# Optimization experiments

Hardware: AMD Instinct MI355X
Metric: run time of the kernel (lower is better)

The kernel has to match this reference:

```python
import jax, jax.numpy as jnp
import numpy as np

SHIFT = 1  # fixed value of the random shift_direction in the original __init__


def _unfold_k3(x, axis):
    """Extract length-3 patches (zero pad 1 each side) along `axis`.
    Inserts a new kernel axis of size 3 right after `axis` (c-major, kh-minor),
    matching torch.nn.functional.unfold channel ordering."""
    pad = [(0, 0)] * x.ndim
    pad[axis] = (1, 1)
    xp = jnp.pad(x, pad)
    L = x.shape[axis]
    sl = lambda i: jax.lax.slice_in_dim(xp, i, i + L, axis=axis)
    return jnp.stack([sl(0), sl(1), sl(2)], axis=axis)


def setup_inputs() -> dict:
    key = jax.random.key(0)
    k1, k2 = jax.random.split(key)
    x = jax.random.normal(k1, (1024, 64, 28, 28), dtype=jnp.float32)
    W = jax.random.normal(k2, (32, 3, 3, 128), dtype=jnp.float32)
    return {"x": x, "W": W}


def reference(x, W):
    # shift along width
    t = jnp.roll(x, SHIFT, axis=3)                        # (1024,64,28,28)
    # merge (C,H) -> pseudo-channel, unfold k=3 along original W (im2col #1)
    t = t.reshape(1024, 1792, 28)
    t = _unfold_k3(t, axis=2)                             # (1024,1792,3,28) = (n, c*h, kh, w)
    t = t.reshape(1024, 64, 28, 3, 28)                    # (n, c, h, kh, w)
    # split channels into 2 groups, interleave with w, shifted group-mix sum
    t = t.reshape(1024, 2, 32, 28, 3, 28)
    t = jnp.transpose(t, (0, 2, 3, 4, 5, 1))              # (n, 32, h, kh, w, 2)
    t = t.reshape(1024, 32, 28, 3, 56)
    t = jnp.roll(t, SHIFT, axis=4)
    t = t.reshape(1024, 32, 28, 3, 28, 2).sum(axis=5)     # (n, 32, h, kh, w)
    t = jnp.transpose(t, (0, 1, 2, 4, 3))                 # (n, 32, h, w, kh)
    # second unfold k=3 along h (im2col #2)
    t = t.reshape(1024, 32, 28, 84)                       # (n, 32, h, w*kh)
    t = _unfold_k3(t, axis=2)                             # (n, 32, kh2, h, w*kh)
    t = t.reshape(1024, 32, 3, 28, 28, 3)                 # (n, l, j, h, w, k)
    t = jnp.transpose(t, (0, 1, 3, 2, 4, 5))              # (m, l, n, j, o, k)
    # 3x3 conv as einsum: 32 in-ch -> 128 out-ch
    y = jnp.einsum('mlnjok,ljki->mnoi', t, W)             # (1024,28,28,128)
    return jnp.transpose(y, (0, 3, 1, 2))                 # (1024,128,28,28)
```

## Files before the change

kernel.cpp:

```cpp
#include <hip/hip_runtime.h>
#include <hip/hip_bf16.h>

typedef __attribute__((ext_vector_type(8))) short short8;
typedef __attribute__((ext_vector_type(4))) float float4v;

#define HH 28
#define WD 28
#define CIN 64
#define COUT 128
#define KTOT 288

__global__ __launch_bounds__(256) void prep_w_kernel(const float* __restrict__ W,
                                                     __hip_bfloat16* __restrict__ Wbf) {
    int idx = blockIdx.x * 256 + threadIdx.x;
    if (idx >= COUT * KTOT) return;
    int i = idx / KTOT;
    int K = idx - i * KTOT;
    int jk = K >> 5;
    int l = K & 31;
    int j = jk / 3;
    int k = jk - j * 3;
    Wbf[idx] = __float2bfloat16(W[((l * 3 + j) * 3 + k) * COUT + i]);
}

__global__ __launch_bounds__(256) void conv_kernel(const float* __restrict__ x,
                                                   const __hip_bfloat16* __restrict__ Wbf,
                                                   float* __restrict__ out) {
    __shared__ __align__(16) char Vb[30 * 30 * 64];
    __shared__ __align__(16) char V0b[30 * 3 * 64];

    const int m = blockIdx.x;
    const int tid = threadIdx.x;
    const float* xm = x + (size_t)m * (CIN * HH * WD);

    for (int idx = tid; idx < 30 * 4 * 32; idx += 256) {
        int a  = idx & 31;
        int lq = (idx >> 5) & 3;
        int rp = idx >> 7;
        if (a >= 30) continue;
        int r = rp - 1;
        bool rok = (r >= 0) && (r < HH);
        bool m1 = rok && (a < 28);
        bool m2 = rok && (a >= 1) && (a <= 28);
        int i1 = a - 1; if (i1 < 0) i1 += 28;
        int i2 = a - 2; if (i2 < 0) i2 += 28;
        const float* x1 = xm + ((lq * 8) * HH + r) * WD;
        const float* x2 = x1 + 32 * HH * WD;
        short8 sv;
#pragma unroll
        for (int c = 0; c < 8; ++c) {
            float t = 0.f;
            if (m1) t += x1[c * HH * WD + i1];
            if (m2) t += x2[c * HH * WD + i2];
            __hip_bfloat16 hb = __float2bfloat16(t);
            sv[c] = *reinterpret_cast<short*>(&hb);
        }
        unsigned byte = (unsigned)(rp * 30 + a) * 64 + (unsigned)lq * 16;
        byte ^= (byte >> 3) & 0x30;
        *(short8*)(Vb + byte) = sv;
    }

    for (int idx = tid; idx < 30 * 3 * 32; idx += 256) {
        int l = idx & 31;
        int t3 = idx >> 5;
        int k = t3 % 3;
        int rp = t3 / 3;
        int r = rp - 1;
        float v = 0.f;
        if (r >= 0 && r < HH) {
            const float* x1 = xm + (l * HH + r) * WD;
            const float* x2 = x1 + 32 * HH * WD;
            if (k == 0) v = x2[25];
            else if (k == 1) v = x1[27] + x2[26];
            else v = x1[0];
        }
        __hip_bfloat16 hb = __float2bfloat16(v);
        *(__hip_bfloat16*)(V0b + idx * 2) = hb;
    }
    __syncthreads();

    const int lane = tid & 63;
    const int wv = tid >> 6;
    const int row = lane & 15;
    const int q = lane >> 4;
    const unsigned qb = (unsigned)q * 16;

    short8 Areg[2][9];
#pragma unroll
    for (int mt = 0; mt < 2; ++mt) {
        const __hip_bfloat16* ap = Wbf + (wv * 32 + mt * 16 + row) * KTOT + q * 8;
#pragma unroll
        for (int s = 0; s < 9; ++s)
            Areg[mt][s] = *(const short8*)(ap + s * 32);
    }

    const bool spec0 = (row == 0);
    const bool spec1 = (row >= 12);

    for (int h = 0; h < HH; ++h) {
        float4v acc[2][2] = {};
#pragma unroll
        for (int s = 0; s < 9; ++s) {
            const int j = s / 3;
            const int k = s - j * 3;
            const int rp = h + j;
            int a0 = row + k - 1;
            unsigned b0 = (unsigned)((rp * 30 + a0) * 64) + qb;
            b0 ^= (b0 >> 3) & 0x30;
            const char* p0 = spec0 ? (V0b + (unsigned)(rp * 3 + k) * 64 + qb)
                                   : (Vb + b0);
            unsigned b1 = (unsigned)((rp * 30 + (row + 15 + k)) * 64) + qb;
            b1 ^= (b1 >> 3) & 0x30;
            const char* p1 = spec1 ? (V0b + qb) : (Vb + b1);

            short8 bfr0 = *(const short8*)p0;
            short8 bfr1 = *(const short8*)p1;

            acc[0][0] = __builtin_amdgcn_mfma_f32_16x16x32_bf16(Areg[0][s], bfr0, acc[0][0], 0, 0, 0);
            acc[1][0] = __builtin_amdgcn_mfma_f32_16x16x32_bf16(Areg[1][s], bfr0, acc[1][0], 0, 0, 0);
            acc[0][1] = __builtin_amdgcn_mfma_f32_16x16x32_bf16(Areg[0][s], bfr1, acc[0][1], 0, 0, 0);
            acc[1][1] = __builtin_amdgcn_mfma_f32_16x16x32_bf16(Areg[1][s], bfr1, acc[1][1], 0, 0, 0);
        }
#pragma unroll
        for (int mt = 0; mt < 2; ++mt) {
            const int ibase = wv * 32 + mt * 16 + q * 4;
            float* op0 = out + (((size_t)m * COUT + ibase) * HH + h) * WD;
#pragma unroll
            for (int rr = 0; rr < 4; ++rr) {
                op0[rr * (HH * WD) + row] = acc[mt][0][rr];
                if (row < 12) op0[rr * (HH * WD) + 16 + row] = acc[mt][1][rr];
            }
        }
    }
}

extern "C" void kernel_launch(void* const* d_in, const int* in_sizes, int n_in,
                              void* d_out, int out_size, void* d_ws, size_t ws_size,
                              hipStream_t stream) {
    const float* x = (const float*)d_in[0];
    const float* W = (const float*)d_in[1];
    float* out = (float*)d_out;
    __hip_bfloat16* Wbf = (__hip_bfloat16*)d_ws;

    prep_w_kernel<<<(COUT * KTOT + 255) / 256, 256, 0, stream>>>(W, Wbf);
    conv_kernel<<<1024, 256, 0, stream>>>(x, Wbf, out);
}
```

Baseline: 803.2 us.

## Split each image's rows across two blocks to shrink LDS and raise occupancy

Each block now handles 14 of the 28 output rows of one image, staging only the 16 padded input rows it needs, so LDS per block drops from about 63KB to about 34KB. This is meant to let more blocks fit per CU (launch bounds hint 4) and give the GPU twice as many blocks. The weight register load is hoisted above the LDS staging so its latency overlaps, and a small zero region replaces reuse of the V0 buffer for padding. The cost is redundant staging of the two halo rows per block and duplicated weight loads.

```diff
diff --git a/kernel.cpp b/kernel.cpp
--- a/kernel.cpp
+++ b/kernel.cpp
@@ -9,6 +9,11 @@
 #define CIN 64
 #define COUT 128
 #define KTOT 288
+#define HB 14
+#define RP 16
+#define V0OFF (RP * 30 * 64)
+#define ZOFF  (V0OFF + RP * 3 * 64)
+#define LDSZ  (ZOFF + 64)
 
 __global__ __launch_bounds__(256) void prep_w_kernel(const float* __restrict__ W,
                                                      __hip_bfloat16* __restrict__ Wbf) {
@@ -23,61 +28,15 @@
     Wbf[idx] = __float2bfloat16(W[((l * 3 + j) * 3 + k) * COUT + i]);
 }
 
-__global__ __launch_bounds__(256) void conv_kernel(const float* __restrict__ x,
-                                                   const __hip_bfloat16* __restrict__ Wbf,
-                                                   float* __restrict__ out) {
-    __shared__ __align__(16) char Vb[30 * 30 * 64];
-    __shared__ __align__(16) char V0b[30 * 3 * 64];
+__global__ __launch_bounds__(256, 4) void conv_kernel(const float* __restrict__ x,
+                                                      const __hip_bfloat16* __restrict__ Wbf,
+                                                      float* __restrict__ out) {
+    __shared__ __align__(16) char L[LDSZ];
 
-    const int m = blockIdx.x;
+    const int hb = blockIdx.x;
+    const int m  = blockIdx.y;
     const int tid = threadIdx.x;
     const float* xm = x + (size_t)m * (CIN * HH * WD);
-
-    for (int idx = tid; idx < 30 * 4 * 32; idx += 256) {
-        int a  = idx & 31;
-        int lq = (idx >> 5) & 3;
-        int rp = idx >> 7;
-        if (a >= 30) continue;
-        int r = rp - 1;
-        bool rok = (r >= 0) && (r < HH);
-        bool m1 = rok && (a < 28);
-        bool m2 = rok && (a >= 1) && (a <= 28);
-        int i1 = a - 1; if (i1 < 0) i1 += 28;
-        int i2 = a - 2; if (i2 < 0) i2 += 28;
-        const float* x1 = xm + ((lq * 8) * HH + r) * WD;
-        const float* x2 = x1 + 32 * HH * WD;
-        short8 sv;
-#pragma unroll
-        for (int c = 0; c < 8; ++c) {
-            float t = 0.f;
-            if (m1) t += x1[c * HH * WD + i1];
-            if (m2) t += x2[c * HH * WD + i2];
-            __hip_bfloat16 hb = __float2bfloat16(t);
-            sv[c] = *reinterpret_cast<short*>(&hb);
-        }
-        unsigned byte = (unsigned)(rp * 30 + a) * 64 + (unsigned)lq * 16;
-        byte ^= (byte >> 3) & 0x30;
-        *(short8*)(Vb + byte) = sv;
-    }
-
-    for (int idx = tid; idx < 30 * 3 * 32; idx += 256) {
-        int l = idx & 31;
-        int t3 = idx >> 5;
-        int k = t3 % 3;
-        int rp = t3 / 3;
-        int r = rp - 1;
-        float v = 0.f;
-        if (r >= 0 && r < HH) {
-            const float* x1 = xm + (l * HH + r) * WD;
-            const float* x2 = x1 + 32 * HH * WD;
-            if (k == 0) v = x2[25];
-            else if (k == 1) v = x1[27] + x2[26];
-            else v = x1[0];
-        }
-        __hip_bfloat16 hb = __float2bfloat16(v);
-        *(__hip_bfloat16*)(V0b + idx * 2) = hb;
-    }
-    __syncthreads();
 
     const int lane = tid & 63;
     const int wv = tid >> 6;
@@ -94,33 +53,82 @@
             Areg[mt][s] = *(const short8*)(ap + s * 32);
     }
 
+    if (tid < 16) *(float*)(L + ZOFF + tid * 4) = 0.f;
+
+    for (int idx = tid; idx < RP * 4 * 32; idx += 256) {
+        int a  = idx & 31;
+        int lq = (idx >> 5) & 3;
+        int rp = idx >> 7;
+        if (a < 30) {
+            int r = hb * HB + rp - 1;
+            bool rok = (r >= 0) && (r < HH);
+            bool m1 = rok && (a < 28);
+            bool m2 = rok && (a >= 1) && (a <= 28);
+            int i1 = a - 1; if (i1 < 0) i1 += 28;
+            int i2 = a - 2; if (i2 < 0) i2 += 28;
+            const float* x1 = xm + ((lq * 8) * HH + r) * WD;
+            const float* x2 = x1 + 32 * HH * WD;
+            short8 sv;
+#pragma unroll
+            for (int c = 0; c < 8; ++c) {
+                float t = 0.f;
+                if (m1) t += x1[c * HH * WD + i1];
+                if (m2) t += x2[c * HH * WD + i2];
+                __hip_bfloat16 hv = __float2bfloat16(t);
+                sv[c] = *reinterpret_cast<short*>(&hv);
+            }
+            unsigned byte = (unsigned)(rp * 30 + a) * 64 + (unsigned)lq * 16;
+            byte ^= (byte >> 3) & 0x30;
+            *(short8*)(L + byte) = sv;
+        }
+    }
+
+    for (int idx = tid; idx < RP * 3 * 32; idx += 256) {
+        int l = idx & 31;
+        int t3 = idx >> 5;
+        int k = t3 % 3;
+        int rp = t3 / 3;
+        int r = hb * HB + rp - 1;
+        float v = 0.f;
+        if (r >= 0 && r < HH) {
+            const float* x1 = xm + (l * HH + r) * WD;
+            const float* x2 = x1 + 32 * HH * WD;
+            if (k == 0) v = x2[25];
+            else if (k == 1) v = x1[27] + x2[26];
+            else v = x1[0];
+        }
+        __hip_bfloat16 hv = __float2bfloat16(v);
+        *(__hip_bfloat16*)(L + V0OFF + idx * 2) = hv;
+    }
+    __syncthreads();
+
     const bool spec0 = (row == 0);
     const bool spec1 = (row >= 12);
 
-    for (int h = 0; h < HH; ++h) {
+    for (int hl = 0; hl < HB; ++hl) {
         float4v acc[2][2] = {};
 #pragma unroll
         for (int s = 0; s < 9; ++s) {
             const int j = s / 3;
             const int k = s - j * 3;
-            const int rp = h + j;
+            const int rp = hl + j;
             int a0 = row + k - 1;
             unsigned b0 = (unsigned)((rp * 30 + a0) * 64) + qb;
             b0 ^= (b0 >> 3) & 0x30;
-            const char* p0 = spec0 ? (V0b + (unsigned)(rp * 3 + k) * 64 + qb)
-                                   : (Vb + b0);
+            unsigned off0 = spec0 ? (unsigned)(V0OFF + (rp * 3 + k) * 64) + qb : b0;
             unsigned b1 = (unsigned)((rp * 30 + (row + 15 + k)) * 64) + qb;
             b1 ^= (b1 >> 3) & 0x30;
-            const char* p1 = spec1 ? (V0b + qb) : (Vb + b1);
+            unsigned off1 = spec1 ? (unsigned)ZOFF + qb : b1;
 
-            short8 bfr0 = *(const short8*)p0;
-            short8 bfr1 = *(const short8*)p1;
+            short8 bfr0 = *(const short8*)(L + off0);
+            short8 bfr1 = *(const short8*)(L + off1);
 
             acc[0][0] = __builtin_amdgcn_mfma_f32_16x16x32_bf16(Areg[0][s], bfr0, acc[0][0], 0, 0, 0);
             acc[1][0] = __builtin_amdgcn_mfma_f32_16x16x32_bf16(Areg[1][s], bfr0, acc[1][0], 0, 0, 0);
             acc[0][1] = __builtin_amdgcn_mfma_f32_16x16x32_bf16(Areg[0][s], bfr1, acc[0][1], 0, 0, 0);
             acc[1][1] = __builtin_amdgcn_mfma_f32_16x16x32_bf16(Areg[1][s], bfr1, acc[1][1], 0, 0, 0);
         }
+        const int h = hb * HB + hl;
 #pragma unroll
         for (int mt = 0; mt < 2; ++mt) {
             const int ibase = wv * 32 + mt * 16 + q * 4;
@@ -143,5 +151,5 @@
     __hip_bfloat16* Wbf = (__hip_bfloat16*)d_ws;
 
     prep_w_kernel<<<(COUT * KTOT + 255) / 256, 256, 0, stream>>>(W, Wbf);
-    conv_kernel<<<1024, 256, 0, stream>>>(x, Wbf, out);
+    conv_kernel<<<dim3(2, 1024), 256, 0, stream>>>(x, Wbf, out);
 }
```

After: 749.1 us. -6.7%, faster.

## Stream input rows via async global-to-LDS loads into a rolling ring buffer

Applied to the files above, without the earlier changes.

Replaces the up-front staging of the whole 30x30 padded input tile with a 4-slot ring buffer. One wave issues async global_load_lds for upcoming input rows, and the other waves build the bf16 mixed rows from LDS a few rows ahead of the MFMA loop. This shrinks LDS use so more blocks fit per CU (launch bounds set to 4) and overlaps global loads with compute. The cost is a barrier per output row and a load-issuing wave whose stalls sit on the critical path.

```diff
diff --git a/kernel.cpp b/kernel.cpp
--- a/kernel.cpp
+++ b/kernel.cpp
@@ -9,6 +9,16 @@
 #define CIN 64
 #define COUT 128
 #define KTOT 288
+
+#define VOFF  0
+#define V0OFF 7680
+#define ZOFF  (V0OFF + 768)
+#define XOFF  (ZOFF + 64)
+#define XROW  7168
+#define LDSZ  (XOFF + 4 * XROW)
+
+typedef const __attribute__((address_space(1))) char gchar;
+typedef __attribute__((address_space(3))) char lchar;
 
 __global__ __launch_bounds__(256) void prep_w_kernel(const float* __restrict__ W,
                                                      __hip_bfloat16* __restrict__ Wbf) {
@@ -23,112 +33,150 @@
     Wbf[idx] = __float2bfloat16(W[((l * 3 + j) * 3 + k) * COUT + i]);
 }
 
-__global__ __launch_bounds__(256) void conv_kernel(const float* __restrict__ x,
-                                                   const __hip_bfloat16* __restrict__ Wbf,
-                                                   float* __restrict__ out) {
-    __shared__ __align__(16) char Vb[30 * 30 * 64];
-    __shared__ __align__(16) char V0b[30 * 3 * 64];
+__global__ __launch_bounds__(256, 4) void conv_kernel(const float* __restrict__ x,
+                                                      const __hip_bfloat16* __restrict__ Wbf,
+                                                      float* __restrict__ out) {
+    __shared__ __align__(16) char L[LDSZ];
+    char* Lb = (char*)L;
 
     const int m = blockIdx.x;
     const int tid = threadIdx.x;
     const float* xm = x + (size_t)m * (CIN * HH * WD);
 
-    for (int idx = tid; idx < 30 * 4 * 32; idx += 256) {
-        int a  = idx & 31;
-        int lq = (idx >> 5) & 3;
-        int rp = idx >> 7;
-        if (a >= 30) continue;
-        int r = rp - 1;
-        bool rok = (r >= 0) && (r < HH);
-        bool m1 = rok && (a < 28);
-        bool m2 = rok && (a >= 1) && (a <= 28);
-        int i1 = a - 1; if (i1 < 0) i1 += 28;
-        int i2 = a - 2; if (i2 < 0) i2 += 28;
-        const float* x1 = xm + ((lq * 8) * HH + r) * WD;
-        const float* x2 = x1 + 32 * HH * WD;
-        short8 sv;
-#pragma unroll
-        for (int c = 0; c < 8; ++c) {
-            float t = 0.f;
-            if (m1) t += x1[c * HH * WD + i1];
-            if (m2) t += x2[c * HH * WD + i2];
-            __hip_bfloat16 hb = __float2bfloat16(t);
-            sv[c] = *reinterpret_cast<short*>(&hb);
-        }
-        unsigned byte = (unsigned)(rp * 30 + a) * 64 + (unsigned)lq * 16;
-        byte ^= (byte >> 3) & 0x30;
-        *(short8*)(Vb + byte) = sv;
-    }
-
-    for (int idx = tid; idx < 30 * 3 * 32; idx += 256) {
-        int l = idx & 31;
-        int t3 = idx >> 5;
-        int k = t3 % 3;
-        int rp = t3 / 3;
-        int r = rp - 1;
-        float v = 0.f;
-        if (r >= 0 && r < HH) {
-            const float* x1 = xm + (l * HH + r) * WD;
-            const float* x2 = x1 + 32 * HH * WD;
-            if (k == 0) v = x2[25];
-            else if (k == 1) v = x1[27] + x2[26];
-            else v = x1[0];
-        }
-        __hip_bfloat16 hb = __float2bfloat16(v);
-        *(__hip_bfloat16*)(V0b + idx * 2) = hb;
-    }
-    __syncthreads();
-
     const int lane = tid & 63;
     const int wv = tid >> 6;
-    const int row = lane & 15;
+    const int wrow = lane & 15;
     const int q = lane >> 4;
     const unsigned qb = (unsigned)q * 16;
+
+    if (tid < 16) *(float*)(Lb + ZOFF + tid * 4) = 0.f;
 
     short8 Areg[2][9];
 #pragma unroll
     for (int mt = 0; mt < 2; ++mt) {
-        const __hip_bfloat16* ap = Wbf + (wv * 32 + mt * 16 + row) * KTOT + q * 8;
+        const __hip_bfloat16* ap = Wbf + (wv * 32 + mt * 16 + wrow) * KTOT + q * 8;
 #pragma unroll
         for (int s = 0; s < 9; ++s)
             Areg[mt][s] = *(const short8*)(ap + s * 32);
     }
 
-    const bool spec0 = (row == 0);
-    const bool spec1 = (row >= 12);
+    auto stage_row = [&](int r) {
+        if (wv == 3 && r < HH) {
+            char* dst = Lb + XOFF + (unsigned)(r & 3) * XROW;
+#pragma unroll
+            for (int t = 0; t < 7; ++t) {
+                int fi = t * 256 + lane * 4;
+                int ch = fi / 28;
+                int w = fi - ch * 28;
+                const float* gsrc = xm + (ch * HH + r) * WD + w;
+                __builtin_amdgcn_global_load_lds((gchar*)(const char*)gsrc,
+                                                 (lchar*)(dst + t * 1024), 16, 0, 0);
+            }
+        }
+    };
+
+    auto build_row = [&](int rp) {
+        int r = rp - 1;
+        bool rok = (r >= 0) && (r < HH);
+        unsigned xbase = XOFF + (unsigned)(r & 3) * XROW;
+        const float* xr = (const float*)(Lb + xbase);
+        if (tid < 128) {
+            int a = tid & 31;
+            int lq = tid >> 5;
+            bool m1 = rok && (a < 28);
+            bool m2 = rok && (a >= 1) && (a <= 28);
+            int i1 = a - 1; if (i1 < 0) i1 += 28;
+            int i2 = a - 2; if (i2 < 0) i2 += 28;
+            short8 sv;
+#pragma unroll
+            for (int c = 0; c < 8; ++c) {
+                int ch = lq * 8 + c;
+                float t1 = m1 ? xr[ch * WD + i1] : 0.f;
+                float t2 = m2 ? xr[(ch + 32) * WD + i2] : 0.f;
+                __hip_bfloat16 hv = __float2bfloat16(t1 + t2);
+                sv[c] = *reinterpret_cast<short*>(&hv);
+            }
+            if (a < 30) {
+                unsigned byte = (unsigned)((((rp & 3) * 30 + a) * 64) + lq * 16);
+                byte ^= (byte >> 3) & 0x30;
+                *(short8*)(Lb + byte) = sv;
+            }
+        } else if (tid < 192) {
+#pragma unroll
+            for (int e0 = 0; e0 < 2; ++e0) {
+                int e = (tid - 128) + e0 * 64;
+                if (e < 96) {
+                    int k = e >> 5;
+                    int l = e & 31;
+                    float v = 0.f;
+                    if (rok) {
+                        if (k == 0) v = xr[(l + 32) * WD + 25];
+                        else if (k == 1) v = xr[l * WD + 27] + xr[(l + 32) * WD + 26];
+                        else v = xr[l * WD + 0];
+                    }
+                    __hip_bfloat16 hv = __float2bfloat16(v);
+                    *(__hip_bfloat16*)(Lb + V0OFF +
+                        (unsigned)((((rp & 3) * 3 + k) * 64) + l * 2)) = hv;
+                }
+            }
+        }
+    };
+
+    stage_row(0); stage_row(1); stage_row(2); stage_row(3);
+    if (wv == 3) asm volatile("s_waitcnt vmcnt(0)" ::: "memory");
+    __syncthreads();
+    build_row(0); build_row(1); build_row(2);
+    __syncthreads();
+
+    asm volatile(""
+        : "+v"(Areg[0][0]), "+v"(Areg[0][1]), "+v"(Areg[0][2]), "+v"(Areg[0][3]),
+          "+v"(Areg[0][4]), "+v"(Areg[0][5]), "+v"(Areg[0][6]), "+v"(Areg[0][7]),
+          "+v"(Areg[0][8]),
+          "+v"(Areg[1][0]), "+v"(Areg[1][1]), "+v"(Areg[1][2]), "+v"(Areg[1][3]),
+          "+v"(Areg[1][4]), "+v"(Areg[1][5]), "+v"(Areg[1][6]), "+v"(Areg[1][7]),
+          "+v"(Areg[1][8]));
+
+    const bool spec0 = (wrow == 0);
+    const bool spec1 = (wrow >= 12);
 
     for (int h = 0; h < HH; ++h) {
+        stage_row(h + 4);
+        if (h <= 26) build_row(h + 3);
+
         float4v acc[2][2] = {};
 #pragma unroll
         for (int s = 0; s < 9; ++s) {
             const int j = s / 3;
             const int k = s - j * 3;
-            const int rp = h + j;
-            int a0 = row + k - 1;
-            unsigned b0 = (unsigned)((rp * 30 + a0) * 64) + qb;
+            const unsigned slot = (unsigned)((h + j) & 3);
+            int a0 = wrow + k - 1;
+            unsigned b0 = (unsigned)(((int)(slot * 30) + a0) * 64) + qb;
             b0 ^= (b0 >> 3) & 0x30;
-            const char* p0 = spec0 ? (V0b + (unsigned)(rp * 3 + k) * 64 + qb)
-                                   : (Vb + b0);
-            unsigned b1 = (unsigned)((rp * 30 + (row + 15 + k)) * 64) + qb;
+            unsigned off0 = spec0 ? (unsigned)(V0OFF + (slot * 3 + k) * 64) + qb : b0;
+            unsigned b1 = (unsigned)((slot * 30 + (unsigned)(wrow + 15 + k)) * 64) + qb;
             b1 ^= (b1 >> 3) & 0x30;
-            const char* p1 = spec1 ? (V0b + qb) : (Vb + b1);
+            unsigned off1 = spec1 ? (unsigned)ZOFF + qb : b1;
 
-            short8 bfr0 = *(const short8*)p0;
-            short8 bfr1 = *(const short8*)p1;
+            short8 bfr0 = *(const short8*)(Lb + off0);
+            short8 bfr1 = *(const short8*)(Lb + off1);
 
             acc[0][0] = __builtin_amdgcn_mfma_f32_16x16x32_bf16(Areg[0][s], bfr0, acc[0][0], 0, 0, 0);
             acc[1][0] = __builtin_amdgcn_mfma_f32_16x16x32_bf16(Areg[1][s], bfr0, acc[1][0], 0, 0, 0);
             acc[0][1] = __builtin_amdgcn_mfma_f32_16x16x32_bf16(Areg[0][s], bfr1, acc[0][1], 0, 0, 0);
             acc[1][1] = __builtin_amdgcn_mfma_f32_16x16x32_bf16(Areg[1][s], bfr1, acc[1][1], 0, 0, 0);
         }
+
+        if (wv == 3) asm volatile("s_waitcnt vmcnt(0)" ::: "memory");
+        __syncthreads();
+
 #pragma unroll
         for (int mt = 0; mt < 2; ++mt) {
             const int ibase = wv * 32 + mt * 16 + q * 4;
             float* op0 = out + (((size_t)m * COUT + ibase) * HH + h) * WD;
 #pragma unroll
             for (int rr = 0; rr < 4; ++rr) {
-                op0[rr * (HH * WD) + row] = acc[mt][0][rr];
-                if (row < 12) op0[rr * (HH * WD) + 16 + row] = acc[mt][1][rr];
+                op0[rr * (HH * WD) + wrow] = acc[mt][0][rr];
+                if (wrow < 12) op0[rr * (HH * WD) + 16 + wrow] = acc[mt][1][rr];
             }
         }
     }
```

After: 777.1 us. 1.03x faster.
